# Kernel optimization log

Measured on AMD Instinct MI355X. Metric: run time of the kernel, lower is better.

The kernel has to match this reference:

```python
import jax, jax.numpy as jnp
import numpy as np
import math

HID = 768
HEADS = 12
HEAD_DIM = HID // HEADS
B, L = 64, 1024


def _xavier(key, shape):
    fan_in, fan_out = shape[0], shape[1]
    lim = math.sqrt(6.0 / (fan_in + fan_out))
    return jax.random.uniform(key, shape, jnp.float32, -lim, lim)


def setup_inputs() -> dict:
    key = jax.random.key(0)
    ks = jax.random.split(key, 12)
    inp = {
        "x_img": jax.random.normal(ks[0], (B, L, HID), jnp.float32),
        "cond": jax.random.normal(ks[1], (B, HID), jnp.float32),
        # attention projections
        "wq": _xavier(ks[2], (HID, HID)), "bq": jnp.zeros((HID,), jnp.float32),
        "wk": _xavier(ks[3], (HID, HID)), "bk": jnp.zeros((HID,), jnp.float32),
        "wv": _xavier(ks[4], (HID, HID)), "bv": jnp.zeros((HID,), jnp.float32),
        "wo": _xavier(ks[5], (HID, HID)), "bo": jnp.zeros((HID,), jnp.float32),
        # adaLN: zero-initialized in the original (keep small random so grads are non-trivial? No — stay faithful: zero init is the module's init, but zero would kill modulation. Use small random for a meaningful test.)
        "w_ada": jax.random.normal(ks[6], (HID, 6 * HID), jnp.float32) * 0.02,
        "b_ada": jnp.zeros((6 * HID,), jnp.float32),
        # MLP
        "w1": _xavier(ks[7], (HID, HID)), "b1": jnp.zeros((HID,), jnp.float32),
        "w2": _xavier(ks[8], (HID, HID)), "b2": jnp.zeros((HID,), jnp.float32),
        # LayerNorm params (norm_1: default scale=1, bias init const 1; norm_2: scale init const 1, bias default 0)
        "ln1_scale": jnp.ones((HID,), jnp.float32), "ln1_bias": jnp.ones((HID,), jnp.float32),
        "ln2_scale": jnp.ones((HID,), jnp.float32), "ln2_bias": jnp.zeros((HID,), jnp.float32),
    }
    return inp


def _layernorm(x, scale, bias, eps=1e-6):
    mu = jnp.mean(x, axis=-1, keepdims=True)
    var = jnp.var(x, axis=-1, keepdims=True)
    return (x - mu) * jax.lax.rsqrt(var + eps) * scale + bias


def _modulate(x, shift, scale):
    # shift/scale: [B, H] -> broadcast over seq axis
    return x * (1.0 + scale[:, None, :]) + shift[:, None, :]


def _attention(x, wq, bq, wk, bk, wv, bv, wo, bo):
    q = x @ wq + bq
    k = x @ wk + bk
    v = x @ wv + bv
    def split(t):
        b, l, _ = t.shape
        return t.reshape(b, l, HEADS, HEAD_DIM).transpose(0, 2, 1, 3)  # b h l d
    q, k, v = split(q), split(k), split(v)
    logits = jnp.einsum("bhqd,bhkd->bhqk", q, k) / math.sqrt(HEAD_DIM)
    attn = jax.nn.softmax(logits, axis=-1)
    out = jnp.einsum("bhqk,bhkd->bhqd", attn, v)
    out = out.transpose(0, 2, 1, 3).reshape(x.shape)  # b l (h d)
    return out @ wo + bo


def reference(x_img, cond, wq, bq, wk, bk, wv, bv, wo, bo, w_ada, b_ada,
              w1, b1, w2, b2, ln1_scale, ln1_bias, ln2_scale, ln2_bias):
    c = jax.nn.silu(cond) @ w_ada + b_ada  # [B, 6H]
    shift_msa, scale_msa, gate_msa, shift_mlp, scale_mlp, gate_mlp = jnp.split(c, 6, axis=1)

    h = _modulate(_layernorm(x_img, ln1_scale, ln1_bias), shift_msa, scale_msa)
    attn_out = _attention(h, wq, bq, wk, bk, wv, bv, wo, bo)
    x = x_img + gate_msa[:, None, :] * attn_out

    h2 = _modulate(_layernorm(x, ln2_scale, ln2_bias), shift_mlp, scale_mlp)
    mlp_out = jax.nn.silu(h2 @ w1 + b1) @ w2 + b2
    x = x + gate_mlp[:, None, :] * mlp_out
    return x
```

## Files before the change

kernel.cpp:

```cpp
#include <hip/hip_runtime.h>
#include <hip/hip_bf16.h>

typedef __bf16 bf16x8 __attribute__((ext_vector_type(8)));
typedef __bf16 bf16x4 __attribute__((ext_vector_type(4)));
typedef float  f32x4  __attribute__((ext_vector_type(4)));

#define MFMA_BF16(A_, B_, C_) __builtin_amdgcn_mfma_f32_16x16x32_bf16(A_, B_, C_, 0, 0, 0)

static constexpr int    HIDC  = 768;
static constexpr int    BB    = 64;
static constexpr int    LL    = 1024;
static constexpr int    MROWS = BB * LL;
static constexpr int    NHEAD = 12;
static constexpr int    HD    = 64;
static constexpr size_t QKV1  = (size_t)BB * NHEAD * LL * HD;
static constexpr float  QSCALE = 0.1803368801111204f;

static constexpr size_t OFF_WQKVT = 0;
static constexpr size_t OFF_WOT   = OFF_WQKVT + (size_t)2304 * 768 * 2;
static constexpr size_t OFF_W1T   = OFF_WOT   + (size_t)768 * 768 * 2;
static constexpr size_t OFF_W2T   = OFF_W1T   + (size_t)768 * 768 * 2;
static constexpr size_t OFF_BQKV  = OFF_W2T   + (size_t)768 * 768 * 2;
static constexpr size_t OFF_C     = OFF_BQKV  + (size_t)2304 * 4;
static constexpr size_t OFF_H     = OFF_C     + (size_t)64 * 4608 * 4;
static constexpr size_t OFF_AO    = OFF_H     + (size_t)MROWS * HIDC * 2;
static constexpr size_t OFF_QKV   = OFF_AO    + (size_t)MROWS * HIDC * 2;

__device__ __forceinline__ void async16(const __bf16* g, __bf16* l) {
    __builtin_amdgcn_global_load_lds((const __attribute__((address_space(1))) void*)g,
                                     (__attribute__((address_space(3))) void*)l, 16, 0, 0);
}

#define PH_BARRIER() do { __builtin_amdgcn_sched_barrier(0); asm volatile("" ::: "memory"); \
    __builtin_amdgcn_s_barrier(); asm volatile("" ::: "memory"); __builtin_amdgcn_sched_barrier(0); } while (0)

__global__ __launch_bounds__(256) void tcvt6_k(const float* __restrict__ s0, const float* __restrict__ s1,
                                               const float* __restrict__ s2, const float* __restrict__ s3,
                                               const float* __restrict__ s4, const float* __restrict__ s5,
                                               __bf16* __restrict__ dbase) {
    __shared__ float t[64][65];
    const int bid = blockIdx.x;
    const int widx = bid / 144;
    const int tb = bid - widx * 144;
    const int kt = tb / 12, nt = tb - kt * 12;
    const float* src = (widx == 0) ? s0 : (widx == 1) ? s1 : (widx == 2) ? s2
                     : (widx == 3) ? s3 : (widx == 4) ? s4 : s5;
    const int tid = threadIdx.x;
    const int r = tid >> 4, c4 = (tid & 15) * 4;
    #pragma unroll
    for (int i = 0; i < 4; ++i) {
        const float4 v = *(const float4*)(src + (size_t)(kt * 64 + r + 16 * i) * 768 + nt * 64 + c4);
        t[r + 16 * i][c4 + 0] = v.x; t[r + 16 * i][c4 + 1] = v.y;
        t[r + 16 * i][c4 + 2] = v.z; t[r + 16 * i][c4 + 3] = v.w;
    }
    __syncthreads();
    const int n = tid >> 2, kg = (tid & 3) * 8;
    #pragma unroll
    for (int i = 0; i < 2; ++i) {
        const int k = kg + i * 32;
        bf16x8 o;
        #pragma unroll
        for (int j = 0; j < 8; ++j) o[j] = (__bf16)t[k + j][n];
        *(bf16x8*)(dbase + (size_t)widx * 768 * 768 + (size_t)(nt * 64 + n) * 768 + kt * 64 + k) = o;
    }
}

__global__ __launch_bounds__(256) void bcat_k(const float* __restrict__ bq, const float* __restrict__ bk,
                                              const float* __restrict__ bv, float* __restrict__ bqkv) {
    int i = blockIdx.x * 256 + threadIdx.x;
    if (i < 2304) {
        int w = i / 768, r = i - w * 768;
        const float* p = (w == 0) ? bq : (w == 1) ? bk : bv;
        bqkv[i] = p[r];
    }
}

__global__ __launch_bounds__(256) void ada_k(const float* __restrict__ cond, const float* __restrict__ w_ada,
                                             const float* __restrict__ b_ada, float* __restrict__ c) {
    __shared__ float s[8][768];
    const int tid = threadIdx.x;
    const int bt = blockIdx.x / 18;
    const int nt = blockIdx.x % 18;
    #pragma unroll
    for (int i = 0; i < 24; ++i) {
        int idx = i * 256 + tid;
        int bb = idx / 768, kk = idx - bb * 768;
        float v = cond[(size_t)(bt * 8 + bb) * 768 + kk];
        s[bb][kk] = v / (1.f + __expf(-v));
    }
    __syncthreads();
    const int n = nt * 256 + tid;
    float acc[8];
    #pragma unroll
    for (int j = 0; j < 8; ++j) acc[j] = 0.f;
    for (int k = 0; k < 768; ++k) {
        float w = w_ada[(size_t)k * 4608 + n];
        #pragma unroll
        for (int j = 0; j < 8; ++j) acc[j] += s[j][k] * w;
    }
    float bias = b_ada[n];
    #pragma unroll
    for (int j = 0; j < 8; ++j) c[(size_t)(bt * 8 + j) * 4608 + n] = acc[j] + bias;
}

__global__ __launch_bounds__(256) void ln_mod_k(const float* __restrict__ x,
                                                const float* __restrict__ lns, const float* __restrict__ lnb,
                                                const float* __restrict__ c, int shift_off, int scale_off,
                                                __bf16* __restrict__ out) {
    const int row = blockIdx.x, tid = threadIdx.x;
    const size_t base = (size_t)row * HIDC;
    const int b = row >> 10;
    float v0 = x[base + tid], v1 = x[base + 256 + tid], v2 = x[base + 512 + tid];
    float s = v0 + v1 + v2;
    float ss = v0 * v0 + v1 * v1 + v2 * v2;
    #pragma unroll
    for (int off = 1; off < 64; off <<= 1) { s += __shfl_xor(s, off); ss += __shfl_xor(ss, off); }
    __shared__ float red[8];
    const int wave = tid >> 6, lane = tid & 63;
    if (lane == 0) { red[wave] = s; red[4 + wave] = ss; }
    __syncthreads();
    s  = red[0] + red[1] + red[2] + red[3];
    ss = red[4] + red[5] + red[6] + red[7];
    const float mu   = s * (1.f / 768.f);
    const float var  = ss * (1.f / 768.f) - mu * mu;
    const float rstd = rsqrtf(var + 1e-6f);
    const float* cb = c + (size_t)b * 4608;
    #pragma unroll
    for (int i = 0; i < 3; ++i) {
        int col = i * 256 + tid;
        float v = (i == 0) ? v0 : (i == 1) ? v1 : v2;
        float val = (v - mu) * rstd * lns[col] + lnb[col];
        val = val * (1.f + cb[scale_off + col]) + cb[shift_off + col];
        out[base + col] = (__bf16)val;
    }
}

__global__ __launch_bounds__(192) void ln_mod_b_k(const __bf16* __restrict__ x,
                                                  const float* __restrict__ lns, const float* __restrict__ lnb,
                                                  const float* __restrict__ c, int shift_off, int scale_off,
                                                  __bf16* __restrict__ out) {
    const int row = blockIdx.x, tid = threadIdx.x;
    const size_t base = (size_t)row * HIDC;
    const int b = row >> 10;
    const bf16x4 xv = *(const bf16x4*)(x + base + tid * 4);
    float v[4];
    #pragma unroll
    for (int j = 0; j < 4; ++j) v[j] = (float)xv[j];
    float s = v[0] + v[1] + v[2] + v[3];
    float ss = v[0] * v[0] + v[1] * v[1] + v[2] * v[2] + v[3] * v[3];
    #pragma unroll
    for (int off = 1; off < 64; off <<= 1) { s += __shfl_xor(s, off); ss += __shfl_xor(ss, off); }
    __shared__ float red[6];
    const int wave = tid >> 6, lane = tid & 63;
    if (lane == 0) { red[wave] = s; red[3 + wave] = ss; }
    __syncthreads();
    s  = red[0] + red[1] + red[2];
    ss = red[3] + red[4] + red[5];
    const float mu   = s * (1.f / 768.f);
    const float var  = ss * (1.f / 768.f) - mu * mu;
    const float rstd = rsqrtf(var + 1e-6f);
    const float* cb = c + (size_t)b * 4608;
    bf16x4 o;
    #pragma unroll
    for (int j = 0; j < 4; ++j) {
        const int col = tid * 4 + j;
        float val = (v[j] - mu) * rstd * lns[col] + lnb[col];
        val = val * (1.f + cb[scale_off + col]) + cb[shift_off + col];
        o[j] = (__bf16)val;
    }
    *(bf16x4*)(out + base + tid * 4) = o;
}

template<int EPI>
__global__ __launch_bounds__(512, 2) void gemm256_k(const __bf16* __restrict__ A, const __bf16* __restrict__ BT,
                                                    const float* __restrict__ bias, int NBLK,
                                                    const float* __restrict__ e_res, const __bf16* __restrict__ e_resb,
                                                    const float* __restrict__ e_gate, void* __restrict__ out0) {
    constexpr int K = 768;
    constexpr int NKT = K / 64;
    __shared__ __attribute__((aligned(16))) unsigned char LDSB[131072];
    const int tid = threadIdx.x;
    const int nwg = gridDim.x;
    const int cpx = nwg >> 3;
    const int bid = blockIdx.x;
    const int swz = (bid & 7) * cpx + (bid >> 3);
    const int mb = swz / NBLK, nb = swz - mb * NBLK;
    const size_t m0 = (size_t)mb * 256;
    const int n0 = nb * 256;
    const int wave = tid >> 6, lane = tid & 63;
    const int wm = wave >> 2, wn = wave & 3;
    const int lr = lane & 15, lg = lane >> 4;

    int prow[2], pcol[2], pphys[2];
    #pragma unroll
    for (int i = 0; i < 2; ++i) {
        int p = (i * 512 + tid) * 16;
        prow[i]  = p >> 7;
        pcol[i]  = ((p & 127) ^ ((prow[i] & 7) << 4)) >> 1;
        pphys[i] = p;
    }
    auto STAGE = [&](const __bf16* gbase, size_t rowstart, int kt, int regoff) {
        #pragma unroll
        for (int i = 0; i < 2; ++i) {
            const __bf16* g = gbase + (rowstart + (size_t)prow[i]) * K + kt * 64 + pcol[i];
            async16(g, (__bf16*)(LDSB + regoff + pphys[i]));
        }
    };
    auto AFRAG = [&](int db, int mf, int ks) -> bf16x8 {
        const int row = mf * 16 + lr;
        const int ph = row * 128 + ((ks * 64 + lg * 16) ^ ((row & 7) << 4));
        return *(const bf16x8*)(LDSB + db * 65536 + wm * 16384 + ph);
    };
    auto BFRAG = [&](int db, int nf, int ks) -> bf16x8 {
        const int row = (wn & 1) * 64 + nf * 16 + lr;
        const int ph = row * 128 + ((ks * 64 + lg * 16) ^ ((row & 7) << 4));
        return *(const bf16x8*)(LDSB + db * 65536 + 32768 + (wn >> 1) * 16384 + ph);
    };

    f32x4 acc[8][4];
    #pragma unroll
    for (int i = 0; i < 8; ++i)
        #pragma unroll
        for (int j = 0; j < 4; ++j) acc[i][j] = (f32x4){0.f, 0.f, 0.f, 0.f};
    bf16x8 Af[4][2], Af2[4][2], Bf[4][2];

    STAGE(BT, (size_t)n0,       0, 32768);
    STAGE(BT, (size_t)n0 + 128, 0, 49152);
    STAGE(A,  m0,               0, 0);
    STAGE(A,  m0 + 128,         0, 16384);
    STAGE(BT, (size_t)n0,       1, 65536 + 32768);
    STAGE(BT, (size_t)n0 + 128, 1, 65536 + 49152);
    asm volatile("s_waitcnt vmcnt(4)" ::: "memory");
    PH_BARRIER();

    #pragma unroll 2
    for (int g = 0; g < NKT; ++g) {
        const int db = g & 1, dbn = db ^ 1;
        #pragma unroll
        for (int mf = 0; mf < 4; ++mf) { Af[mf][0] = AFRAG(db, mf, 0); Af[mf][1] = AFRAG(db, mf, 1); }
        #pragma unroll
        for (int nf = 0; nf < 2; ++nf) { Bf[nf][0] = BFRAG(db, nf, 0); Bf[nf][1] = BFRAG(db, nf, 1); }
        if (g + 1 < NKT) STAGE(A, m0, g + 1, dbn * 65536);
        #pragma unroll
        for (int nf = 2; nf < 4; ++nf) { Bf[nf][0] = BFRAG(db, nf, 0); Bf[nf][1] = BFRAG(db, nf, 1); }
        __builtin_amdgcn_s_setprio(1);
        #pragma unroll
        for (int ks = 0; ks < 2; ++ks)
            #pragma unroll
            for (int mf = 0; mf < 4; ++mf)
                #pragma unroll
                for (int nf = 0; nf < 2; ++nf)
                    acc[mf][nf] = MFMA_BF16(Af[mf][ks], Bf[nf][ks], acc[mf][nf]);
        __builtin_amdgcn_s_setprio(0);
        PH_BARRIER();
        if (g + 1 < NKT) STAGE(A, m0 + 128, g + 1, dbn * 65536 + 16384);
        #pragma unroll
        for (int mf = 0; mf < 4; ++mf) { Af2[mf][0] = AFRAG(db, mf + 4, 0); Af2[mf][1] = AFRAG(db, mf + 4, 1); }
        __builtin_amdgcn_s_setprio(1);
        #pragma unroll
        for (int ks = 0; ks < 2; ++ks)
            #pragma unroll
            for (int mf = 0; mf < 4; ++mf)
                #pragma unroll
                for (int nf = 2; nf < 4; ++nf)
                    acc[mf][nf] = MFMA_BF16(Af[mf][ks], Bf[nf][ks], acc[mf][nf]);
        __builtin_amdgcn_s_setprio(0);
        PH_BARRIER();
        if (g + 2 < NKT) STAGE(BT, (size_t)n0, g + 2, db * 65536 + 32768);
        __builtin_amdgcn_s_setprio(1);
        #pragma unroll
        for (int ks = 0; ks < 2; ++ks)
            #pragma unroll
            for (int mf = 0; mf < 4; ++mf)
                #pragma unroll
                for (int nf = 0; nf < 2; ++nf)
                    acc[mf + 4][nf] = MFMA_BF16(Af2[mf][ks], Bf[nf][ks], acc[mf + 4][nf]);
        __builtin_amdgcn_s_setprio(0);
        PH_BARRIER();
        if (g + 2 < NKT) STAGE(BT, (size_t)n0 + 128, g + 2, db * 65536 + 49152);
        __builtin_amdgcn_s_setprio(1);
        #pragma unroll
        for (int ks = 0; ks < 2; ++ks)
            #pragma unroll
            for (int mf = 0; mf < 4; ++mf)
                #pragma unroll
                for (int nf = 2; nf < 4; ++nf)
                    acc[mf + 4][nf] = MFMA_BF16(Af2[mf][ks], Bf[nf][ks], acc[mf + 4][nf]);
        __builtin_amdgcn_s_setprio(0);
        if (g < NKT - 2)       asm volatile("s_waitcnt vmcnt(4)" ::: "memory");
        else if (g == NKT - 2) asm volatile("s_waitcnt vmcnt(0)" ::: "memory");
        if (g + 1 < NKT) PH_BARRIER();
    }

    #pragma unroll
    for (int mf = 0; mf < 8; ++mf) {
        #pragma unroll
        for (int nf = 0; nf < 4; ++nf) {
            const int col = wn * 64 + nf * 16 + lr;
            const int n = n0 + col;
            const int row0 = wm * 128 + mf * 16 + lg * 4;
            const size_t mbase = m0 + row0;
            float v4[4];
            #pragma unroll
            for (int r = 0; r < 4; ++r) v4[r] = acc[mf][nf][r] + bias[n];
            if constexpr (EPI == 0) {
                const int which = n / 768, rem = n - which * 768;
                const int hh = rem >> 6, dd = rem & 63;
                const size_t bI = mbase >> 10;
                const size_t lI0 = mbase & 1023;
                if (which == 0) {
                    #pragma unroll
                    for (int r = 0; r < 4; ++r)
                        ((__bf16*)out0)[(((size_t)bI * NHEAD + hh) * LL + lI0 + r) * HD + dd] = (__bf16)(v4[r] * QSCALE);
                } else if (which == 1) {
                    #pragma unroll
                    for (int r = 0; r < 4; ++r)
                        ((__bf16*)out0)[QKV1 + (((size_t)bI * NHEAD + hh) * LL + lI0 + r) * HD + dd] = (__bf16)v4[r];
                } else {
                    const int tile = (int)(lI0 >> 6), kv = (int)(lI0 & 63);
                    const int ks = kv >> 5, r5 = kv & 31;
                    const int lgj = (r5 >> 2) & 3;
                    const int jb = (r5 >> 4) << 2;
                    const int of = dd >> 4, lr2 = dd & 15;
                    bf16x4 pk;
                    #pragma unroll
                    for (int r = 0; r < 4; ++r) pk[r] = (__bf16)v4[r];
                    *(bf16x4*)((__bf16*)out0 + 2 * QKV1 + ((size_t)bI * NHEAD + hh) * (LL * HD)
                               + (size_t)tile * 4096 + ((ks * 4 + of) * 64 + lgj * 16 + lr2) * 8 + jb) = pk;
                }
            } else {
                #pragma unroll
                for (int r = 0; r < 4; ++r) {
                    const size_t m = mbase + r;
                    if constexpr (EPI == 2) {
                        float sv = v4[r] / (1.f + __expf(-v4[r]));
                        ((__bf16*)out0)[m * HIDC + n] = (__bf16)sv;
                    } else if constexpr (EPI == 3) {
                        size_t bI = m >> 10;
                        float gg = e_gate[bI * 4608 + n];
                        ((__bf16*)out0)[m * HIDC + n] = (__bf16)(e_res[m * HIDC + n] + gg * v4[r]);
                    } else {
                        size_t bI = m >> 10;
                        float gg = e_gate[bI * 4608 + n];
                        ((float*)out0)[m * HIDC + n] = (float)e_resb[m * HIDC + n] + gg * v4[r];
                    }
                }
            }
        }
    }
}

__global__ __launch_bounds__(256, 4) void attn_k(const __bf16* __restrict__ qb, const __bf16* __restrict__ kb,
                                                 const __bf16* __restrict__ v2g, __bf16* __restrict__ out) {
    __shared__ __attribute__((aligned(16))) unsigned char LDSA[32768];
    const int nwg = gridDim.x;
    const int cpx = nwg >> 3;
    const int bid = blockIdx.x;
    const int swz = (bid & 7) * cpx + (bid >> 3);
    const int bh = swz >> 3;
    const int qt = swz & 7;
    const int b = bh / NHEAD, h = bh - b * NHEAD;
    const int tid = threadIdx.x;
    const int wave = tid >> 6, lane = tid & 63;
    const int lr = lane & 15, lg = lane >> 4;
    const size_t base = (size_t)bh * LL * HD;

    const int q0 = qt * 128 + wave * 32;
    bf16x8 qf[2][2];
    #pragma unroll
    for (int qi = 0; qi < 2; ++qi) {
        const __bf16* qrow = qb + base + (size_t)(q0 + qi * 16 + lr) * HD;
        qf[qi][0] = *(const bf16x8*)(qrow + lg * 8);
        qf[qi][1] = *(const bf16x8*)(qrow + 32 + lg * 8);
    }
    __builtin_amdgcn_sched_barrier(0);

    int krow[2], kcol[2];
    #pragma unroll
    for (int i = 0; i < 2; ++i) {
        int pp = (i * 256 + tid) * 16;
        krow[i] = pp >> 7;
        kcol[i] = (pp & 127) ^ ((krow[i] & 7) << 4);
    }
    auto STAGE = [&](int t) {
        unsigned char* Lb = LDSA + (t & 1) * 16384;
        const int kv0 = t * 64;
        #pragma unroll
        for (int i = 0; i < 2; ++i) {
            const __bf16* g = kb + base + (size_t)(kv0 + krow[i]) * HD + (kcol[i] >> 1);
            async16(g, (__bf16*)(Lb + (i * 256 + tid) * 16));
        }
        #pragma unroll
        for (int i = 0; i < 2; ++i) {
            int pp = (i * 256 + tid) * 16;
            const __bf16* g = v2g + base + (size_t)t * 4096 + (pp >> 1);
            async16(g, (__bf16*)(Lb + 8192 + pp));
        }
    };

    bf16x8 vones;
    #pragma unroll
    for (int j = 0; j < 8; ++j) vones[j] = (__bf16)1.0f;

    f32x4 acc[2][4];
    f32x4 accl[2];
    #pragma unroll
    for (int qi = 0; qi < 2; ++qi) {
        accl[qi] = (f32x4){0.f, 0.f, 0.f, 0.f};
        #pragma unroll
        for (int i = 0; i < 4; ++i) acc[qi][i] = (f32x4){0.f, 0.f, 0.f, 0.f};
    }

    STAGE(0);

    for (int t = 0; t < LL / 64; ++t) {
        asm volatile("s_waitcnt vmcnt(0)" ::: "memory");
        PH_BARRIER();
        if (t + 1 < LL / 64) STAGE(t + 1);
        const unsigned char* KB = LDSA + (t & 1) * 16384;
        const unsigned char* VB = KB + 8192;

        f32x4 s[2][4];
        #pragma unroll
        for (int sf = 0; sf < 4; ++sf) {
            const int row = sf * 16 + lr;
            const bf16x8 kf0 = *(const bf16x8*)(KB + row * 128 + ((lg * 16) ^ ((row & 7) << 4)));
            const bf16x8 kf1 = *(const bf16x8*)(KB + row * 128 + ((64 + lg * 16) ^ ((row & 7) << 4)));
            #pragma unroll
            for (int qi = 0; qi < 2; ++qi) {
                f32x4 tt = (f32x4){0.f, 0.f, 0.f, 0.f};
                tt = MFMA_BF16(kf0, qf[qi][0], tt);
                tt = MFMA_BF16(kf1, qf[qi][1], tt);
                s[qi][sf] = tt;
            }
        }
        #pragma unroll
        for (int ks = 0; ks < 2; ++ks) {
            bf16x8 pb[2];
            #pragma unroll
            for (int qi = 0; qi < 2; ++qi) {
                #pragma unroll
                for (int j = 0; j < 4; ++j) {
                    pb[qi][j]     = (__bf16)exp2f(s[qi][2 * ks][j]);
                    pb[qi][4 + j] = (__bf16)exp2f(s[qi][2 * ks + 1][j]);
                }
                accl[qi] = MFMA_BF16(vones, pb[qi], accl[qi]);
            }
            #pragma unroll
            for (int of = 0; of < 4; ++of) {
                const bf16x8 vf = *(const bf16x8*)(VB + ((ks * 4 + of) * 64 + lane) * 16);
                #pragma unroll
                for (int qi = 0; qi < 2; ++qi)
                    acc[qi][of] = MFMA_BF16(vf, pb[qi], acc[qi][of]);
            }
        }
    }
    #pragma unroll
    for (int qi = 0; qi < 2; ++qi) {
        const float inv = 1.f / accl[qi][0];
        const int qq = q0 + qi * 16 + lr;
        #pragma unroll
        for (int of = 0; of < 4; ++of)
            #pragma unroll
            for (int r = 0; r < 4; ++r) {
                const int d = of * 16 + lg * 4 + r;
                out[((size_t)b * LL + qq) * HIDC + h * HD + d] = (__bf16)(acc[qi][of][r] * inv);
            }
    }
}

extern "C" void kernel_launch(void* const* d_in, const int* in_sizes, int n_in,
                              void* d_out, int out_size, void* d_ws, size_t ws_size,
                              hipStream_t stream) {
    const float* x_img = (const float*)d_in[0];
    const float* cond  = (const float*)d_in[1];
    const float* wq    = (const float*)d_in[2];
    const float* bq    = (const float*)d_in[3];
    const float* wk    = (const float*)d_in[4];
    const float* bk    = (const float*)d_in[5];
    const float* wv    = (const float*)d_in[6];
    const float* bv    = (const float*)d_in[7];
    const float* wo    = (const float*)d_in[8];
    const float* bo    = (const float*)d_in[9];
    const float* w_ada = (const float*)d_in[10];
    const float* b_ada = (const float*)d_in[11];
    const float* w1    = (const float*)d_in[12];
    const float* b1    = (const float*)d_in[13];
    const float* w2    = (const float*)d_in[14];
    const float* b2    = (const float*)d_in[15];
    const float* ln1s  = (const float*)d_in[16];
    const float* ln1b  = (const float*)d_in[17];
    const float* ln2s  = (const float*)d_in[18];
    const float* ln2b  = (const float*)d_in[19];

    char* ws = (char*)d_ws;
    __bf16* wqkvT = (__bf16*)(ws + OFF_WQKVT);
    __bf16* woT   = (__bf16*)(ws + OFF_WOT);
    __bf16* w1T   = (__bf16*)(ws + OFF_W1T);
    __bf16* w2T   = (__bf16*)(ws + OFF_W2T);
    float*  bqkv  = (float*)(ws + OFF_BQKV);
    float*  cbuf  = (float*)(ws + OFF_C);
    __bf16* hbuf  = (__bf16*)(ws + OFF_H);
    __bf16* aobuf = (__bf16*)(ws + OFF_AO);
    __bf16* qkv   = (__bf16*)(ws + OFF_QKV);
    __bf16* xbuf  = (__bf16*)(ws + OFF_QKV);

    dim3 blk(256);
    dim3 blk512(512);

    tcvt6_k<<<6 * 144, blk, 0, stream>>>(wq, wk, wv, wo, w1, w2, wqkvT);
    bcat_k<<<9, blk, 0, stream>>>(bq, bk, bv, bqkv);
    ada_k<<<144, blk, 0, stream>>>(cond, w_ada, b_ada, cbuf);

    ln_mod_k<<<MROWS, blk, 0, stream>>>(x_img, ln1s, ln1b, cbuf, 0, 768, hbuf);

    gemm256_k<0><<<2304, blk512, 0, stream>>>(hbuf, wqkvT, bqkv, 9, nullptr, nullptr, nullptr, (void*)qkv);

    attn_k<<<BB * NHEAD * 8, blk, 0, stream>>>(qkv, qkv + QKV1, qkv + 2 * QKV1, aobuf);

    gemm256_k<3><<<768, blk512, 0, stream>>>(aobuf, woT, bo, 3, x_img, nullptr, cbuf + 2 * 768, (void*)xbuf);

    ln_mod_b_k<<<MROWS, dim3(192), 0, stream>>>(xbuf, ln2s, ln2b, cbuf, 3 * 768, 4 * 768, hbuf);

    gemm256_k<2><<<768, blk512, 0, stream>>>(hbuf, w1T, b1, 3, nullptr, nullptr, nullptr, (void*)aobuf);

    gemm256_k<4><<<768, blk512, 0, stream>>>(aobuf, w2T, b2, 3, nullptr, xbuf, cbuf + 5 * 768, d_out);

    (void)in_sizes; (void)n_in; (void)out_size; (void)ws_size;
}
```

Before: 1.105 ms.

## Enlarge attention workgroups to 256 queries and vectorize layernorm and output stores

The attention kernel now uses 512-thread workgroups covering 256 query rows per head, with half as many workgroups. Each K/V tile staged into LDS is therefore reused by twice as many waves, and each thread issues one async copy per tile instead of two. The first layernorm kernel switches to 192 threads that load float4 and store bf16x4 vectors. The attention epilogue also writes bf16x4 vectors instead of scalar stores. The launch bound of 8 workgroups of 512 threads per CU may force register limits that cause spills, and fewer workgroups means coarser load balance across CUs.

Result: slower. 2.829 ms (+156.0%).

```diff
diff --git a/kernel.cpp b/kernel.cpp
--- a/kernel.cpp
+++ b/kernel.cpp
@@ -103,36 +103,38 @@
     for (int j = 0; j < 8; ++j) c[(size_t)(bt * 8 + j) * 4608 + n] = acc[j] + bias;
 }
 
-__global__ __launch_bounds__(256) void ln_mod_k(const float* __restrict__ x,
-                                                const float* __restrict__ lns, const float* __restrict__ lnb,
-                                                const float* __restrict__ c, int shift_off, int scale_off,
-                                                __bf16* __restrict__ out) {
+__global__ __launch_bounds__(192) void ln_mod_f4_k(const float* __restrict__ x,
+                                                   const float* __restrict__ lns, const float* __restrict__ lnb,
+                                                   const float* __restrict__ c, int shift_off, int scale_off,
+                                                   __bf16* __restrict__ out) {
     const int row = blockIdx.x, tid = threadIdx.x;
     const size_t base = (size_t)row * HIDC;
     const int b = row >> 10;
-    float v0 = x[base + tid], v1 = x[base + 256 + tid], v2 = x[base + 512 + tid];
-    float s = v0 + v1 + v2;
-    float ss = v0 * v0 + v1 * v1 + v2 * v2;
+    const float4 xv = *(const float4*)(x + base + tid * 4);
+    float v[4] = {xv.x, xv.y, xv.z, xv.w};
+    float s = v[0] + v[1] + v[2] + v[3];
+    float ss = v[0] * v[0] + v[1] * v[1] + v[2] * v[2] + v[3] * v[3];
     #pragma unroll
     for (int off = 1; off < 64; off <<= 1) { s += __shfl_xor(s, off); ss += __shfl_xor(ss, off); }
-    __shared__ float red[8];
+    __shared__ float red[6];
     const int wave = tid >> 6, lane = tid & 63;
-    if (lane == 0) { red[wave] = s; red[4 + wave] = ss; }
+    if (lane == 0) { red[wave] = s; red[3 + wave] = ss; }
     __syncthreads();
-    s  = red[0] + red[1] + red[2] + red[3];
-    ss = red[4] + red[5] + red[6] + red[7];
+    s  = red[0] + red[1] + red[2];
+    ss = red[3] + red[4] + red[5];
     const float mu   = s * (1.f / 768.f);
     const float var  = ss * (1.f / 768.f) - mu * mu;
     const float rstd = rsqrtf(var + 1e-6f);
     const float* cb = c + (size_t)b * 4608;
-    #pragma unroll
-    for (int i = 0; i < 3; ++i) {
-        int col = i * 256 + tid;
-        float v = (i == 0) ? v0 : (i == 1) ? v1 : v2;
-        float val = (v - mu) * rstd * lns[col] + lnb[col];
+    bf16x4 o;
+    #pragma unroll
+    for (int j = 0; j < 4; ++j) {
+        const int col = tid * 4 + j;
+        float val = (v[j] - mu) * rstd * lns[col] + lnb[col];
         val = val * (1.f + cb[scale_off + col]) + cb[shift_off + col];
-        out[base + col] = (__bf16)val;
-    }
+        o[j] = (__bf16)val;
+    }
+    *(bf16x4*)(out + base + tid * 4) = o;
 }
 
 __global__ __launch_bounds__(192) void ln_mod_b_k(const __bf16* __restrict__ x,
@@ -350,22 +352,22 @@
     }
 }
 
-__global__ __launch_bounds__(256, 4) void attn_k(const __bf16* __restrict__ qb, const __bf16* __restrict__ kb,
+__global__ __launch_bounds__(512, 8) void attn_k(const __bf16* __restrict__ qb, const __bf16* __restrict__ kb,
                                                  const __bf16* __restrict__ v2g, __bf16* __restrict__ out) {
     __shared__ __attribute__((aligned(16))) unsigned char LDSA[32768];
     const int nwg = gridDim.x;
     const int cpx = nwg >> 3;
     const int bid = blockIdx.x;
     const int swz = (bid & 7) * cpx + (bid >> 3);
-    const int bh = swz >> 3;
-    const int qt = swz & 7;
+    const int bh = swz >> 2;
+    const int qt = swz & 3;
     const int b = bh / NHEAD, h = bh - b * NHEAD;
     const int tid = threadIdx.x;
     const int wave = tid >> 6, lane = tid & 63;
     const int lr = lane & 15, lg = lane >> 4;
     const size_t base = (size_t)bh * LL * HD;
 
-    const int q0 = qt * 128 + wave * 32;
+    const int q0 = qt * 256 + wave * 32;
     bf16x8 qf[2][2];
     #pragma unroll
     for (int qi = 0; qi < 2; ++qi) {
@@ -375,27 +377,15 @@
     }
     __builtin_amdgcn_sched_barrier(0);
 
-    int krow[2], kcol[2];
-    #pragma unroll
-    for (int i = 0; i < 2; ++i) {
-        int pp = (i * 256 + tid) * 16;
-        krow[i] = pp >> 7;
-        kcol[i] = (pp & 127) ^ ((krow[i] & 7) << 4);
-    }
+    const int pp = tid * 16;
+    const int krow = pp >> 7;
+    const int kcol = (pp & 127) ^ ((krow & 7) << 4);
     auto STAGE = [&](int t) {
         unsigned char* Lb = LDSA + (t & 1) * 16384;
-        const int kv0 = t * 64;
-        #pragma unroll
-        for (int i = 0; i < 2; ++i) {
-            const __bf16* g = kb + base + (size_t)(kv0 + krow[i]) * HD + (kcol[i] >> 1);
-            async16(g, (__bf16*)(Lb + (i * 256 + tid) * 16));
-        }
-        #pragma unroll
-        for (int i = 0; i < 2; ++i) {
-            int pp = (i * 256 + tid) * 16;
-            const __bf16* g = v2g + base + (size_t)t * 4096 + (pp >> 1);
-            async16(g, (__bf16*)(Lb + 8192 + pp));
-        }
+        const __bf16* gk = kb + base + (size_t)(t * 64 + krow) * HD + (kcol >> 1);
+        async16(gk, (__bf16*)(Lb + pp));
+        const __bf16* gv = v2g + base + (size_t)t * 4096 + (pp >> 1);
+        async16(gv, (__bf16*)(Lb + 8192 + pp));
     };
 
     bf16x8 vones;
@@ -460,12 +450,12 @@
         const float inv = 1.f / accl[qi][0];
         const int qq = q0 + qi * 16 + lr;
         #pragma unroll
-        for (int of = 0; of < 4; ++of)
-            #pragma unroll
-            for (int r = 0; r < 4; ++r) {
-                const int d = of * 16 + lg * 4 + r;
-                out[((size_t)b * LL + qq) * HIDC + h * HD + d] = (__bf16)(acc[qi][of][r] * inv);
-            }
+        for (int of = 0; of < 4; ++of) {
+            bf16x4 o;
+            #pragma unroll
+            for (int r = 0; r < 4; ++r) o[r] = (__bf16)(acc[qi][of][r] * inv);
+            *(bf16x4*)(out + ((size_t)b * LL + qq) * HIDC + h * HD + of * 16 + lg * 4) = o;
+        }
     }
 }
 
@@ -506,21 +496,22 @@
     __bf16* xbuf  = (__bf16*)(ws + OFF_QKV);
 
     dim3 blk(256);
+    dim3 blk192(192);
     dim3 blk512(512);
 
     tcvt6_k<<<6 * 144, blk, 0, stream>>>(wq, wk, wv, wo, w1, w2, wqkvT);
     bcat_k<<<9, blk, 0, stream>>>(bq, bk, bv, bqkv);
     ada_k<<<144, blk, 0, stream>>>(cond, w_ada, b_ada, cbuf);
 
-    ln_mod_k<<<MROWS, blk, 0, stream>>>(x_img, ln1s, ln1b, cbuf, 0, 768, hbuf);
+    ln_mod_f4_k<<<MROWS, blk192, 0, stream>>>(x_img, ln1s, ln1b, cbuf, 0, 768, hbuf);
 
     gemm256_k<0><<<2304, blk512, 0, stream>>>(hbuf, wqkvT, bqkv, 9, nullptr, nullptr, nullptr, (void*)qkv);
 
-    attn_k<<<BB * NHEAD * 8, blk, 0, stream>>>(qkv, qkv + QKV1, qkv + 2 * QKV1, aobuf);
+    attn_k<<<BB * NHEAD * 4, blk512, 0, stream>>>(qkv, qkv + QKV1, qkv + 2 * QKV1, aobuf);
 
     gemm256_k<3><<<768, blk512, 0, stream>>>(aobuf, woT, bo, 3, x_img, nullptr, cbuf + 2 * 768, (void*)xbuf);
 
-    ln_mod_b_k<<<MROWS, dim3(192), 0, stream>>>(xbuf, ln2s, ln2b, cbuf, 3 * 768, 4 * 768, hbuf);
+    ln_mod_b_k<<<MROWS, blk192, 0, stream>>>(xbuf, ln2s, ln2b, cbuf, 3 * 768, 4 * 768, hbuf);
 
     gemm256_k<2><<<768, blk512, 0, stream>>>(hbuf, w1T, b1, 3, nullptr, nullptr, nullptr, (void*)aobuf);
 
```
